# Kernel optimization log

Hardware: AMD Instinct MI355X
Metric: run time of the kernel (lower is better)

Reference implementation:

```python
import jax, jax.numpy as jnp
import numpy as np

B, S, D, H = 2, 2048, 2048, 16
DH = D // H
EPS = 1e-5


def layernorm(x, gamma, beta):
    mu = jnp.mean(x, axis=-1, keepdims=True)
    var = jnp.var(x, axis=-1, keepdims=True)
    return (x - mu) * jax.lax.rsqrt(var + EPS) * gamma + beta


def setup_inputs() -> dict:
    key = jax.random.key(0)
    ks = jax.random.split(key, 10)
    sc = 1.0 / np.sqrt(D)
    return {
        "x": jax.random.normal(ks[0], (B, S, D), dtype=jnp.float32),
        "wq": jax.random.normal(ks[1], (D, D), dtype=jnp.float32) * sc,
        "bq": jnp.zeros((D,), jnp.float32),
        "wk": jax.random.normal(ks[2], (D, D), dtype=jnp.float32) * sc,
        "bk": jnp.zeros((D,), jnp.float32),
        "wv": jax.random.normal(ks[3], (D, D), dtype=jnp.float32) * sc,
        "bv": jnp.zeros((D,), jnp.float32),
        "wf": jax.random.normal(ks[4], (D, D), dtype=jnp.float32) * sc,
        "bf": jnp.zeros((D,), jnp.float32),
        "gamma": jnp.ones((D,), jnp.float32),
        "beta": jnp.zeros((D,), jnp.float32),
    }


def reference(x, wq, bq, wk, bk, wv, bv, wf, bf, gamma, beta):
    q = x @ wq + bq
    k = x @ wk + bk
    v = x @ wv + bv
    # split: [B,S,D] -> [B,H,S,DH]
    split = lambda t: t.reshape(B, S, H, DH).transpose(0, 2, 1, 3)
    q, k, v = split(q), split(k), split(v)
    s = jnp.einsum("bhqd,bhkd->bhqk", q, k) / np.sqrt(DH)
    p = jax.nn.softmax(s, axis=-1)
    o = jnp.einsum("bhqk,bhkd->bhqd", p, v)
    # faithful to original buggy concat: flat view of [B,H,S,DH] as [B,S,H*DH]
    o = o.reshape(B, S, H * DH)
    vb = o
    h1 = layernorm(o + x, gamma, beta)
    h2 = h1 @ wf + bf
    out = layernorm(h2 + vb, gamma, beta)
    return out
```

## Files before the change

kernel.cpp:

```cpp
#include <hip/hip_runtime.h>


#define B_ 2
#define S_ 2048
#define D_ 2048
#define H_ 16
#define DH_ 128

typedef __attribute__((ext_vector_type(8))) short s16x8;
typedef __attribute__((ext_vector_type(8))) unsigned short u16x8;
typedef __attribute__((ext_vector_type(4))) float f32x4;
typedef __attribute__((ext_vector_type(4))) unsigned short u16x4;

#define MFMA16(a, b, c) __builtin_amdgcn_mfma_f32_16x16x32_bf16(a, b, c, 0, 0, 0)

__device__ inline unsigned short f2bf(float f) {
  union { float f; unsigned u; } x; x.f = f;
  unsigned r = (x.u + 0x7fffu + ((x.u >> 16) & 1u)) >> 16;
  return (unsigned short)r;
}
__device__ inline float bf2f(unsigned short u) {
  union { unsigned u; float f; } x; x.u = ((unsigned)u) << 16;
  return x.f;
}
__device__ inline unsigned pack2bf(float a, float b) {
  unsigned ua = __builtin_bit_cast(unsigned, a) + 0x8000u;
  unsigned ub = __builtin_bit_cast(unsigned, b) + 0x8000u;
  return __builtin_amdgcn_perm(ub, ua, 0x07060302u);
}

__device__ inline void gld_lds16(const void* g, void* l) {
  __builtin_amdgcn_global_load_lds(
      (__attribute__((address_space(1))) void*)g,
      (__attribute__((address_space(3))) void*)l, 16, 0, 0);
}

__global__ __launch_bounds__(256) void prep_kernel(
    const float* __restrict__ x, unsigned short* __restrict__ xb,
    const float* __restrict__ w0, const float* __restrict__ w1,
    const float* __restrict__ w2, const float* __restrict__ w3,
    unsigned short* __restrict__ o0, unsigned short* __restrict__ o1,
    unsigned short* __restrict__ o2, unsigned short* __restrict__ o3) {
  int z = blockIdx.z;
  int t = threadIdx.x;
  if (z == 4) {
    int base = (blockIdx.y * 32 + blockIdx.x) * 16384 + t * 4;
#pragma unroll
    for (int p = 0; p < 16; ++p) {
      int i = base + p * 1024;
      float4 v = *(const float4*)&x[i];
      u16x4 o;
      o.x = f2bf(v.x); o.y = f2bf(v.y); o.z = f2bf(v.z); o.w = f2bf(v.w);
      *(u16x4*)&xb[i] = o;
    }
    return;
  }
  const float* W = z == 0 ? w0 : z == 1 ? w1 : z == 2 ? w2 : w3;
  unsigned short* WT = z == 0 ? o0 : z == 1 ? o1 : z == 2 ? o2 : o3;
  int n0 = blockIdx.x * 64, k0 = blockIdx.y * 128;
  int cl = t & 15, rw = t >> 4;
  int kb = k0 + rw * 8, nb = n0 + cl * 4;
  float4 f[8];
#pragma unroll
  for (int r = 0; r < 8; ++r) f[r] = *(const float4*)&W[(kb + r) * D_ + nb];
#define TPOSE(comp, i)                                                      \
  {                                                                         \
    u16x8 o = {f2bf(f[0].comp), f2bf(f[1].comp), f2bf(f[2].comp),           \
               f2bf(f[3].comp), f2bf(f[4].comp), f2bf(f[5].comp),           \
               f2bf(f[6].comp), f2bf(f[7].comp)};                           \
    *(u16x8*)&WT[(nb + i) * D_ + kb] = o;                                   \
  }
  TPOSE(x, 0) TPOSE(y, 1) TPOSE(z, 2) TPOSE(w, 3)
#undef TPOSE
}

__global__ __launch_bounds__(256) void gemm_qkv_kernel(
    const unsigned short* __restrict__ A, const unsigned short* __restrict__ W0,
    const unsigned short* __restrict__ W1, const unsigned short* __restrict__ W2,
    const float* __restrict__ b0, const float* __restrict__ b1,
    const float* __restrict__ b2, unsigned short* __restrict__ Qb,
    unsigned short* __restrict__ Kb, unsigned short* __restrict__ Vt,
    float qscale) {
  __shared__ short As[128 * 32];
  __shared__ short Bs[128 * 32];
  int wi = blockIdx.x >> 4;
  int n0 = (blockIdx.x & 15) * 128;
  const unsigned short* BT = wi == 0 ? W0 : wi == 1 ? W1 : W2;
  const float* bias = wi == 0 ? b0 : wi == 1 ? b1 : b2;
  float oscale = wi == 0 ? qscale : 1.0f;

  int t = threadIdx.x, lane = t & 63, w = t >> 6;
  int nl = lane & 15, q = lane >> 4;
  int m0 = blockIdx.y * 128;
  int wr = (w >> 1) * 64, wc = (w & 1) * 64;

  f32x4 acc[4][4];
  f32x4 z4 = {0.f, 0.f, 0.f, 0.f};
#pragma unroll
  for (int i = 0; i < 4; ++i)
#pragma unroll
    for (int j = 0; j < 4; ++j) acc[i][j] = z4;

  for (int kk = 0; kk < 2048; kk += 32) {
    __syncthreads();
#pragma unroll
    for (int i2 = 0; i2 < 2; ++i2) {
      int c = t + 256 * i2;
      int row = c >> 2, dc = c & 3;
      gld_lds16(&A[(m0 + row) * 2048 + kk + dc * 8], &As[c * 8]);
      gld_lds16(&BT[(n0 + row) * 2048 + kk + dc * 8], &Bs[c * 8]);
    }
    __syncthreads();
    s16x8 af[4], bf[4];
#pragma unroll
    for (int i = 0; i < 4; ++i)
      af[i] = *(const s16x8*)&As[(wr + i * 16 + nl) * 32 + q * 8];
#pragma unroll
    for (int j = 0; j < 4; ++j)
      bf[j] = *(const s16x8*)&Bs[(wc + j * 16 + nl) * 32 + q * 8];
#pragma unroll
    for (int i = 0; i < 4; ++i)
#pragma unroll
      for (int j = 0; j < 4; ++j) acc[i][j] = MFMA16(af[i], bf[j], acc[i][j]);
  }
#pragma unroll
  for (int i = 0; i < 4; ++i)
#pragma unroll
    for (int j = 0; j < 4; ++j) {
      int row = m0 + wr + i * 16 + q * 4;
      int col = n0 + wc + j * 16 + nl;
      float bv = bias[col];
      float v[4];
#pragma unroll
      for (int r = 0; r < 4; ++r) v[r] = (acc[i][j][r] + bv) * oscale;
      if (wi == 2) {
        unsigned d0 = pack2bf(v[0], v[1]), d1 = pack2bf(v[2], v[3]);
        long idx = ((long)(((row >> 11) * 16 + (col >> 7)) * 128 + (col & 127))) * 2048 +
                   (row & 2047);
        *(uint2*)&Vt[idx] = (uint2){d0, d1};
      } else {
        unsigned short* out = wi == 0 ? Qb : Kb;
#pragma unroll
        for (int r = 0; r < 4; ++r)
          out[(row + r) * 2048 + col] = f2bf(v[r]);
      }
    }
}

__global__ __launch_bounds__(256, 4) void gemm_ff_kernel(
    const unsigned short* __restrict__ A, const unsigned short* __restrict__ BT,
    const float* __restrict__ bias, unsigned short* __restrict__ Cout) {
  __shared__ short As[128 * 32];
  __shared__ short Bs[64 * 32];
  int t = threadIdx.x, lane = t & 63, w = t >> 6;
  int nl = lane & 15, q = lane >> 4;
  int m0 = blockIdx.y * 128, n0 = blockIdx.x * 64;
  int wr = (w >> 1) * 64, wc = (w & 1) * 32;

  f32x4 acc[4][2];
  f32x4 z4 = {0.f, 0.f, 0.f, 0.f};
#pragma unroll
  for (int i = 0; i < 4; ++i) {
    acc[i][0] = z4;
    acc[i][1] = z4;
  }

  for (int kk = 0; kk < 2048; kk += 32) {
    __syncthreads();
    {
      int c0 = t, c1 = t + 256;
      gld_lds16(&A[(m0 + (c0 >> 2)) * 2048 + kk + (c0 & 3) * 8], &As[c0 * 8]);
      gld_lds16(&A[(m0 + (c1 >> 2)) * 2048 + kk + (c1 & 3) * 8], &As[c1 * 8]);
      gld_lds16(&BT[(n0 + (t >> 2)) * 2048 + kk + (t & 3) * 8], &Bs[t * 8]);
    }
    __syncthreads();
    s16x8 af[4], bf0, bf1;
#pragma unroll
    for (int i = 0; i < 4; ++i)
      af[i] = *(const s16x8*)&As[(wr + i * 16 + nl) * 32 + q * 8];
    bf0 = *(const s16x8*)&Bs[(wc + nl) * 32 + q * 8];
    bf1 = *(const s16x8*)&Bs[(wc + 16 + nl) * 32 + q * 8];
#pragma unroll
    for (int i = 0; i < 4; ++i) {
      acc[i][0] = MFMA16(af[i], bf0, acc[i][0]);
      acc[i][1] = MFMA16(af[i], bf1, acc[i][1]);
    }
  }
#pragma unroll
  for (int i = 0; i < 4; ++i)
#pragma unroll
    for (int j = 0; j < 2; ++j) {
      int row = m0 + wr + i * 16 + q * 4;
      int col = n0 + wc + j * 16 + nl;
      float bv = bias[col];
#pragma unroll
      for (int r = 0; r < 4; ++r)
        Cout[(row + r) * 2048 + col] = f2bf(acc[i][j][r] + bv);
    }
}

__global__ __launch_bounds__(256, 2) void attn_kernel(
    const unsigned short* __restrict__ Q, const unsigned short* __restrict__ K,
    const unsigned short* __restrict__ VT, unsigned short* __restrict__ O) {
  __shared__ short KsA[8192], KsB[8192];
  __shared__ short VsA[8192], VsB[8192];
  __shared__ short Ps[8192];
  int t = threadIdx.x, lane = t & 63, w = t >> 6;
  int nl = lane & 15, q = lane >> 4;
  int bx = blockIdx.x;
  int qb = bx & 15, bh = bx >> 4;
  int b = bh >> 4, h = bh & 15;

  s16x8 qf[2][4];
  int qrow = b * S_ + qb * 128 + w * 32;
#pragma unroll
  for (int t2 = 0; t2 < 2; ++t2)
#pragma unroll
    for (int kc = 0; kc < 4; ++kc)
      qf[t2][kc] = *(const s16x8*)&Q[(qrow + t2 * 16 + nl) * D_ + h * DH_ + kc * 32 + q * 8];

  f32x4 z4 = {0.f, 0.f, 0.f, 0.f};
  f32x4 accO[2][8];
  float m_i[2] = {-1e30f, -1e30f}, l_i[2] = {0.f, 0.f};
#pragma unroll
  for (int t2 = 0; t2 < 2; ++t2)
#pragma unroll
    for (int n8 = 0; n8 < 8; ++n8) accO[t2][n8] = z4;

  int swz = nl & 7;

  const unsigned short* kp[4];
  const unsigned short* vp[4];
#pragma unroll
  for (int i2 = 0; i2 < 4; ++i2) {
    int c = t + 256 * i2;
    int kc = c >> 8, rem = c & 255, s = rem >> 2, dc = rem & 3;
    kp[i2] = K + (long)(b * S_ + s) * D_ + h * DH_ + kc * 32 + dc * 8;
    int d = c >> 3, cp = c & 7, cs = cp ^ (d & 7);
    vp[i2] = VT + (long)(bh * DH_ + d) * S_ + cs * 8;
  }

#define STAGE(bufK, bufV)                           \
  {                                                 \
    _Pragma("unroll") for (int i2 = 0; i2 < 4; ++i2) { \
      gld_lds16(kp[i2], &bufK[(t + 256 * i2) * 8]); \
      gld_lds16(vp[i2], &bufV[(t + 256 * i2) * 8]); \
      kp[i2] += 64 * D_;                            \
      vp[i2] += 64;                                 \
    }                                               \
  }

  auto compute = [&](const short* Ks, const short* Vs) {
    f32x4 accS[2][4];
#pragma unroll
    for (int t2 = 0; t2 < 2; ++t2)
#pragma unroll
      for (int n = 0; n < 4; ++n) accS[t2][n] = z4;
#pragma unroll
    for (int kc = 0; kc < 4; ++kc) {
      s16x8 kf[4];
#pragma unroll
      for (int n = 0; n < 4; ++n)
        kf[n] = *(const s16x8*)&Ks[kc * 2048 + (n * 16 + nl) * 32 + q * 8];
#pragma unroll
      for (int t2 = 0; t2 < 2; ++t2)
#pragma unroll
        for (int n = 0; n < 4; ++n)
          accS[t2][n] = MFMA16(kf[n], qf[t2][kc], accS[t2][n]);
    }

#pragma unroll
    for (int t2 = 0; t2 < 2; ++t2) {
      float mx = -1e30f;
#pragma unroll
      for (int n = 0; n < 4; ++n)
#pragma unroll
        for (int r = 0; r < 4; ++r) mx = fmaxf(mx, accS[t2][n][r]);
      mx = fmaxf(mx, __shfl_xor(mx, 16));
      mx = fmaxf(mx, __shfl_xor(mx, 32));
      float mnew = fmaxf(m_i[t2], mx);
      float alpha = __builtin_amdgcn_exp2f(m_i[t2] - mnew);
      m_i[t2] = mnew;
      float ps = 0.f;
#pragma unroll
      for (int n = 0; n < 4; ++n)
#pragma unroll
        for (int r = 0; r < 4; ++r) {
          float p = __builtin_amdgcn_exp2f(accS[t2][n][r] - mnew);
          accS[t2][n][r] = p;
          ps += p;
        }
      ps += __shfl_xor(ps, 16);
      ps += __shfl_xor(ps, 32);
      l_i[t2] = l_i[t2] * alpha + ps;
      if (__any(alpha < 1.0f)) {
#pragma unroll
        for (int n8 = 0; n8 < 8; ++n8) accO[t2][n8] *= alpha;
      }
      int prow = (w * 32 + t2 * 16 + nl) * 64;
#pragma unroll
      for (int n = 0; n < 4; ++n) {
        unsigned d0 = pack2bf(accS[t2][n][0], accS[t2][n][1]);
        unsigned d1 = pack2bf(accS[t2][n][2], accS[t2][n][3]);
        int c8 = q + 4 * n;
        int off = prow + (((c8 >> 1) ^ swz) * 8 + (c8 & 1) * 4);
        *(uint2*)&Ps[off] = (uint2){d0, d1};
      }
    }

#pragma unroll
    for (int ks = 0; ks < 2; ++ks) {
      s16x8 pf[2];
#pragma unroll
      for (int t2 = 0; t2 < 2; ++t2)
        pf[t2] = *(const s16x8*)&Ps[(w * 32 + t2 * 16 + nl) * 64 + ((4 * ks + q) ^ swz) * 8];
#pragma unroll
      for (int n8 = 0; n8 < 8; ++n8) {
        int d = n8 * 16 + nl;
        int cs = ks * 4 + q;
        int ci = d * 8 + (cs ^ (d & 7));
        s16x8 vf = *(const s16x8*)&Vs[ci * 8];
#pragma unroll
        for (int t2 = 0; t2 < 2; ++t2)
          accO[t2][n8] = MFMA16(vf, pf[t2], accO[t2][n8]);
      }
    }
  };

  STAGE(KsA, VsA);
  for (int it = 0; it < 32; it += 2) {
    __syncthreads();
    STAGE(KsB, VsB);
    compute(KsA, VsA);
    __syncthreads();
    if (it + 2 < 32) STAGE(KsA, VsA);
    compute(KsB, VsB);
  }
#undef STAGE

#pragma unroll
  for (int t2 = 0; t2 < 2; ++t2) {
    float inv = 1.0f / l_i[t2];
    int s = qb * 128 + w * 32 + t2 * 16 + nl;
    unsigned short* orow = &O[((long)(bh * S_ + s)) * DH_];
#pragma unroll
    for (int n8 = 0; n8 < 8; ++n8) {
      unsigned d0 = pack2bf(accO[t2][n8][0] * inv, accO[t2][n8][1] * inv);
      unsigned d1 = pack2bf(accO[t2][n8][2] * inv, accO[t2][n8][3] * inv);
      *(uint2*)&orow[n8 * 16 + q * 4] = (uint2){d0, d1};
    }
  }
}

template <int OUTBF, int INBF>
__global__ __launch_bounds__(256) void ln_kernel(
    const void* __restrict__ Ain, const unsigned short* __restrict__ Ob,
    const float* __restrict__ gamma, const float* __restrict__ beta,
    void* __restrict__ out) {
  int row = blockIdx.x, t = threadIdx.x;
  int lane = t & 63, w = t >> 6;
  float v[8], s = 0.f, s2 = 0.f;
#pragma unroll
  for (int p = 0; p < 8; ++p) {
    int c = t + p * 256;
    float a = INBF ? bf2f(((const unsigned short*)Ain)[row * D_ + c])
                   : ((const float*)Ain)[row * D_ + c];
    a += bf2f(Ob[row * D_ + c]);
    v[p] = a; s += a; s2 += a * a;
  }
#pragma unroll
  for (int mk = 32; mk >= 1; mk >>= 1) {
    s += __shfl_xor(s, mk);
    s2 += __shfl_xor(s2, mk);
  }
  __shared__ float red[8];
  if (lane == 0) { red[w * 2] = s; red[w * 2 + 1] = s2; }
  __syncthreads();
  s = red[0] + red[2] + red[4] + red[6];
  s2 = red[1] + red[3] + red[5] + red[7];
  float mu = s * (1.0f / D_);
  float var = s2 * (1.0f / D_) - mu * mu;
  float rs = rsqrtf(var + 1e-5f);
#pragma unroll
  for (int p = 0; p < 8; ++p) {
    int c = t + p * 256;
    float o = (v[p] - mu) * rs * gamma[c] + beta[c];
    if (OUTBF)
      ((unsigned short*)out)[row * D_ + c] = f2bf(o);
    else
      ((float*)out)[row * D_ + c] = o;
  }
}

extern "C" void kernel_launch(void* const* d_in, const int* in_sizes, int n_in,
                              void* d_out, int out_size, void* d_ws, size_t ws_size,
                              hipStream_t stream) {
  const float* x     = (const float*)d_in[0];
  const float* wq    = (const float*)d_in[1];
  const float* bq    = (const float*)d_in[2];
  const float* wk    = (const float*)d_in[3];
  const float* bk    = (const float*)d_in[4];
  const float* wv    = (const float*)d_in[5];
  const float* bv    = (const float*)d_in[6];
  const float* wf    = (const float*)d_in[7];
  const float* bfb   = (const float*)d_in[8];
  const float* gamma = (const float*)d_in[9];
  const float* beta  = (const float*)d_in[10];

  unsigned short* ws  = (unsigned short*)d_ws;
  unsigned short* WqT = ws;
  unsigned short* WkT = ws + 4194304;
  unsigned short* WvT = ws + 8388608;
  unsigned short* WfT = ws + 12582912;
  unsigned short* Xb  = ws + 16777216;
  unsigned short* Qb  = ws + 25165824;
  unsigned short* Kb  = ws + 33554432;
  unsigned short* Vt  = ws + 41943040;
  unsigned short* Ob  = Xb;
  unsigned short* H1  = Kb;
  unsigned short* H2b = Vt;

  const float scl2 = 0.08838834764831845f * 1.4426950408889634f;

  dim3 blk(256);
  prep_kernel<<<dim3(32, 16, 5), blk, 0, stream>>>(
      x, Xb, wq, wk, wv, wf, WqT, WkT, WvT, WfT);

  gemm_qkv_kernel<<<dim3(48, 32), blk, 0, stream>>>(
      Xb, WqT, WkT, WvT, bq, bk, bv, Qb, Kb, Vt, scl2);

  attn_kernel<<<dim3(512), blk, 0, stream>>>(Qb, Kb, Vt, Ob);

  ln_kernel<1, 0><<<dim3(4096), blk, 0, stream>>>(x, Ob, gamma, beta, (void*)H1);
  gemm_ff_kernel<<<dim3(32, 32), blk, 0, stream>>>(H1, WfT, bfb, H2b);
  ln_kernel<0, 1><<<dim3(4096), blk, 0, stream>>>(H2b, Ob, gamma, beta, d_out);
}
```

Measured before the change: 438.5 us.

## Double GEMM K-tile with swizzled LDS and load attention K straight into registers

Both GEMM kernels now stage 64-wide K slices per barrier instead of 32, with an XOR swizzle on the LDS column chunks to avoid bank conflicts. This halves the number of sync rounds and gives two MFMA sub-steps per tile. The attention kernel drops the K buffers in LDS and prefetches K fragments from global memory into registers for the next tile while the current tile's softmax and PV run. This cuts LDS use and staging traffic, but costs 16 more vector registers and may expose global latency on K.

```diff
diff --git a/kernel.cpp b/kernel.cpp
--- a/kernel.cpp
+++ b/kernel.cpp
@@ -81,8 +81,8 @@
     const float* __restrict__ b2, unsigned short* __restrict__ Qb,
     unsigned short* __restrict__ Kb, unsigned short* __restrict__ Vt,
     float qscale) {
-  __shared__ short As[128 * 32];
-  __shared__ short Bs[128 * 32];
+  __shared__ short As[128 * 64];
+  __shared__ short Bs[128 * 64];
   int wi = blockIdx.x >> 4;
   int n0 = (blockIdx.x & 15) * 128;
   const unsigned short* BT = wi == 0 ? W0 : wi == 1 ? W1 : W2;
@@ -93,6 +93,7 @@
   int nl = lane & 15, q = lane >> 4;
   int m0 = blockIdx.y * 128;
   int wr = (w >> 1) * 64, wc = (w & 1) * 64;
+  int swz = nl & 7;
 
   f32x4 acc[4][4];
   f32x4 z4 = {0.f, 0.f, 0.f, 0.f};
@@ -101,27 +102,32 @@
 #pragma unroll
     for (int j = 0; j < 4; ++j) acc[i][j] = z4;
 
-  for (int kk = 0; kk < 2048; kk += 32) {
-    __syncthreads();
-#pragma unroll
-    for (int i2 = 0; i2 < 2; ++i2) {
+  for (int kk = 0; kk < 2048; kk += 64) {
+    __syncthreads();
+#pragma unroll
+    for (int i2 = 0; i2 < 4; ++i2) {
       int c = t + 256 * i2;
-      int row = c >> 2, dc = c & 3;
+      int row = c >> 3, dc = (c & 7) ^ (row & 7);
       gld_lds16(&A[(m0 + row) * 2048 + kk + dc * 8], &As[c * 8]);
       gld_lds16(&BT[(n0 + row) * 2048 + kk + dc * 8], &Bs[c * 8]);
     }
     __syncthreads();
-    s16x8 af[4], bf[4];
-#pragma unroll
-    for (int i = 0; i < 4; ++i)
-      af[i] = *(const s16x8*)&As[(wr + i * 16 + nl) * 32 + q * 8];
-#pragma unroll
-    for (int j = 0; j < 4; ++j)
-      bf[j] = *(const s16x8*)&Bs[(wc + j * 16 + nl) * 32 + q * 8];
-#pragma unroll
-    for (int i = 0; i < 4; ++i)
-#pragma unroll
-      for (int j = 0; j < 4; ++j) acc[i][j] = MFMA16(af[i], bf[j], acc[i][j]);
+#pragma unroll
+    for (int kc = 0; kc < 2; ++kc) {
+      s16x8 af[4], bf[4];
+#pragma unroll
+      for (int i = 0; i < 4; ++i)
+        af[i] = *(const s16x8*)&As[(wr + i * 16 + nl) * 64 +
+                                   (((kc << 2) + q) ^ swz) * 8];
+#pragma unroll
+      for (int j = 0; j < 4; ++j)
+        bf[j] = *(const s16x8*)&Bs[(wc + j * 16 + nl) * 64 +
+                                   (((kc << 2) + q) ^ swz) * 8];
+#pragma unroll
+      for (int i = 0; i < 4; ++i)
+#pragma unroll
+        for (int j = 0; j < 4; ++j) acc[i][j] = MFMA16(af[i], bf[j], acc[i][j]);
+    }
   }
 #pragma unroll
   for (int i = 0; i < 4; ++i)
@@ -150,12 +156,13 @@
 __global__ __launch_bounds__(256, 4) void gemm_ff_kernel(
     const unsigned short* __restrict__ A, const unsigned short* __restrict__ BT,
     const float* __restrict__ bias, unsigned short* __restrict__ Cout) {
-  __shared__ short As[128 * 32];
-  __shared__ short Bs[64 * 32];
+  __shared__ short As[128 * 64];
+  __shared__ short Bs[64 * 64];
   int t = threadIdx.x, lane = t & 63, w = t >> 6;
   int nl = lane & 15, q = lane >> 4;
   int m0 = blockIdx.y * 128, n0 = blockIdx.x * 64;
   int wr = (w >> 1) * 64, wc = (w & 1) * 32;
+  int swz = nl & 7;
 
   f32x4 acc[4][2];
   f32x4 z4 = {0.f, 0.f, 0.f, 0.f};
@@ -165,25 +172,35 @@
     acc[i][1] = z4;
   }
 
-  for (int kk = 0; kk < 2048; kk += 32) {
-    __syncthreads();
-    {
-      int c0 = t, c1 = t + 256;
-      gld_lds16(&A[(m0 + (c0 >> 2)) * 2048 + kk + (c0 & 3) * 8], &As[c0 * 8]);
-      gld_lds16(&A[(m0 + (c1 >> 2)) * 2048 + kk + (c1 & 3) * 8], &As[c1 * 8]);
-      gld_lds16(&BT[(n0 + (t >> 2)) * 2048 + kk + (t & 3) * 8], &Bs[t * 8]);
-    }
-    __syncthreads();
-    s16x8 af[4], bf0, bf1;
-#pragma unroll
-    for (int i = 0; i < 4; ++i)
-      af[i] = *(const s16x8*)&As[(wr + i * 16 + nl) * 32 + q * 8];
-    bf0 = *(const s16x8*)&Bs[(wc + nl) * 32 + q * 8];
-    bf1 = *(const s16x8*)&Bs[(wc + 16 + nl) * 32 + q * 8];
-#pragma unroll
-    for (int i = 0; i < 4; ++i) {
-      acc[i][0] = MFMA16(af[i], bf0, acc[i][0]);
-      acc[i][1] = MFMA16(af[i], bf1, acc[i][1]);
+  for (int kk = 0; kk < 2048; kk += 64) {
+    __syncthreads();
+#pragma unroll
+    for (int i2 = 0; i2 < 4; ++i2) {
+      int c = t + 256 * i2;
+      int row = c >> 3, dc = (c & 7) ^ (row & 7);
+      gld_lds16(&A[(m0 + row) * 2048 + kk + dc * 8], &As[c * 8]);
+    }
+#pragma unroll
+    for (int i2 = 0; i2 < 2; ++i2) {
+      int c = t + 256 * i2;
+      int row = c >> 3, dc = (c & 7) ^ (row & 7);
+      gld_lds16(&BT[(n0 + row) * 2048 + kk + dc * 8], &Bs[c * 8]);
+    }
+    __syncthreads();
+#pragma unroll
+    for (int kc = 0; kc < 2; ++kc) {
+      s16x8 af[4], bf0, bf1;
+#pragma unroll
+      for (int i = 0; i < 4; ++i)
+        af[i] = *(const s16x8*)&As[(wr + i * 16 + nl) * 64 +
+                                   (((kc << 2) + q) ^ swz) * 8];
+      bf0 = *(const s16x8*)&Bs[(wc + nl) * 64 + (((kc << 2) + q) ^ swz) * 8];
+      bf1 = *(const s16x8*)&Bs[(wc + 16 + nl) * 64 + (((kc << 2) + q) ^ swz) * 8];
+#pragma unroll
+      for (int i = 0; i < 4; ++i) {
+        acc[i][0] = MFMA16(af[i], bf0, acc[i][0]);
+        acc[i][1] = MFMA16(af[i], bf1, acc[i][1]);
+      }
     }
   }
 #pragma unroll
@@ -202,7 +219,6 @@
 __global__ __launch_bounds__(256, 2) void attn_kernel(
     const unsigned short* __restrict__ Q, const unsigned short* __restrict__ K,
     const unsigned short* __restrict__ VT, unsigned short* __restrict__ O) {
-  __shared__ short KsA[8192], KsB[8192];
   __shared__ short VsA[8192], VsB[8192];
   __shared__ short Ps[8192];
   int t = threadIdx.x, lane = t & 63, w = t >> 6;
@@ -229,45 +245,47 @@
 
   int swz = nl & 7;
 
-  const unsigned short* kp[4];
   const unsigned short* vp[4];
 #pragma unroll
   for (int i2 = 0; i2 < 4; ++i2) {
     int c = t + 256 * i2;
-    int kc = c >> 8, rem = c & 255, s = rem >> 2, dc = rem & 3;
-    kp[i2] = K + (long)(b * S_ + s) * D_ + h * DH_ + kc * 32 + dc * 8;
     int d = c >> 3, cp = c & 7, cs = cp ^ (d & 7);
     vp[i2] = VT + (long)(bh * DH_ + d) * S_ + cs * 8;
   }
-
-#define STAGE(bufK, bufV)                           \
-  {                                                 \
+  const unsigned short* kbp = K + (long)(b * S_) * D_ + (long)nl * D_ + h * DH_ + q * 8;
+
+  s16x8 kf[4][4];
+  auto kfload = [&](int kv) {
+#pragma unroll
+    for (int kc = 0; kc < 4; ++kc)
+#pragma unroll
+      for (int n = 0; n < 4; ++n)
+        kf[kc][n] = *(const s16x8*)&kbp[(long)(kv + n * 16) * D_ + kc * 32];
+  };
+
+#define STAGEV(buf)                                    \
+  {                                                    \
     _Pragma("unroll") for (int i2 = 0; i2 < 4; ++i2) { \
-      gld_lds16(kp[i2], &bufK[(t + 256 * i2) * 8]); \
-      gld_lds16(vp[i2], &bufV[(t + 256 * i2) * 8]); \
-      kp[i2] += 64 * D_;                            \
-      vp[i2] += 64;                                 \
-    }                                               \
-  }
-
-  auto compute = [&](const short* Ks, const short* Vs) {
+      gld_lds16(vp[i2], &buf[(t + 256 * i2) * 8]);     \
+      vp[i2] += 64;                                    \
+    }                                                  \
+  }
+
+  auto tile = [&](const short* Vs, int nextkv) {
     f32x4 accS[2][4];
 #pragma unroll
     for (int t2 = 0; t2 < 2; ++t2)
 #pragma unroll
       for (int n = 0; n < 4; ++n) accS[t2][n] = z4;
 #pragma unroll
-    for (int kc = 0; kc < 4; ++kc) {
-      s16x8 kf[4];
-#pragma unroll
-      for (int n = 0; n < 4; ++n)
-        kf[n] = *(const s16x8*)&Ks[kc * 2048 + (n * 16 + nl) * 32 + q * 8];
+    for (int kc = 0; kc < 4; ++kc)
 #pragma unroll
       for (int t2 = 0; t2 < 2; ++t2)
 #pragma unroll
         for (int n = 0; n < 4; ++n)
-          accS[t2][n] = MFMA16(kf[n], qf[t2][kc], accS[t2][n]);
-    }
+          accS[t2][n] = MFMA16(kf[kc][n], qf[t2][kc], accS[t2][n]);
+
+    kfload(nextkv);
 
 #pragma unroll
     for (int t2 = 0; t2 < 2; ++t2) {
@@ -327,16 +345,17 @@
     }
   };
 
-  STAGE(KsA, VsA);
+  STAGEV(VsA);
+  kfload(0);
   for (int it = 0; it < 32; it += 2) {
     __syncthreads();
-    STAGE(KsB, VsB);
-    compute(KsA, VsA);
-    __syncthreads();
-    if (it + 2 < 32) STAGE(KsA, VsA);
-    compute(KsB, VsB);
-  }
-#undef STAGE
+    STAGEV(VsB);
+    tile(VsA, (it + 1) * 64);
+    __syncthreads();
+    if (it + 2 < 32) STAGEV(VsA);
+    tile(VsB, (it + 2 < 32 ? it + 2 : 31) * 64);
+  }
+#undef STAGEV
 
 #pragma unroll
   for (int t2 = 0; t2 < 2; ++t2) {
```

Measured after the change: 581.0 us. 1.32x slower.
